# Kernel tuning notes

Hardware: AMD Instinct MI355X
Metric: run time of the kernel (lower is better)

Reference implementation:

```python
import jax, jax.numpy as jnp
import numpy as np

BATCH_SIZE = 8192   # args.batch_size
NUM_VIEWS = 2       # args.num_views
TEMPERATURE = 0.07  # args.loss_args['temperature']
FEAT_DIM = 256
N = (BATCH_SIZE // 2) * NUM_VIEWS  # rows of features


def _static_index_maps():
    # labels = sorted cat of num_views copies of arange(batch_size//2)
    labels = np.sort(np.tile(np.arange(BATCH_SIZE // 2), NUM_VIEWS))
    lab_mat = labels[None, :] == labels[:, None]          # (N, N) bool
    # off-diagonal column indices: for row i, columns [0..N-1] excluding i,
    # in ascending order (matches torch boolean-mask extraction order)
    j = np.arange(N - 1)
    cols = j[None, :] + (j[None, :] >= np.arange(N)[:, None])  # (N, N-1)
    lab_off = np.take_along_axis(lab_mat, cols, axis=1)        # (N, N-1) bool
    k = NUM_VIEWS - 1  # positives per row
    # stable sort puts positive positions first, preserving column order
    order = np.argsort(~lab_off, axis=1, kind='stable')
    pos_cols = order[:, :k]   # (N, k)
    neg_cols = order[:, k:]   # (N, N-1-k)
    return cols, pos_cols, neg_cols

_COLS, _POS_COLS, _NEG_COLS = _static_index_maps()


def setup_inputs() -> dict:
    key = jax.random.key(0)
    features = jax.random.normal(key, (N, FEAT_DIM), dtype=jnp.float32)
    return {"features": features}


def reference(features):
    # L2 normalize rows (F.normalize eps clamp)
    norm = jnp.maximum(jnp.linalg.norm(features, axis=1, keepdims=True), 1e-12)
    f = features / norm
    sim = f @ f.T                                            # (N, N)
    sim_off = jnp.take_along_axis(sim, jnp.asarray(_COLS), axis=1)       # (N, N-1)
    positives = jnp.take_along_axis(sim_off, jnp.asarray(_POS_COLS), axis=1)
    negatives = jnp.take_along_axis(sim_off, jnp.asarray(_NEG_COLS), axis=1)
    logits = jnp.concatenate([positives, negatives], axis=1) / TEMPERATURE
    # CrossEntropyLoss with target class 0 for every row
    loss = jnp.mean(-jax.nn.log_softmax(logits, axis=1)[:, 0])
    return loss
```

## Files before the change

### kernel.cpp

```cpp
#include <hip/hip_runtime.h>
#include <stdint.h>

#define N_ROWS 8192
#define FEAT   256
#define YSPLIT 32
#define CPB    (N_ROWS / YSPLIT)

typedef __bf16 bf16x8 __attribute__((ext_vector_type(8)));
typedef float  f32x4  __attribute__((ext_vector_type(4)));

__device__ __forceinline__ unsigned short f2bf(float x) {
    union { float f; uint32_t u; } v; v.f = x;
    uint32_t u = v.u;
    return (unsigned short)((u + 0x7FFFu + ((u >> 16) & 1u)) >> 16);
}

__global__ void knorm(const float* __restrict__ feat,
                      unsigned short* __restrict__ fb,
                      float* __restrict__ pos) {
    __shared__ float ex[4][FEAT];
    int wave = threadIdx.x >> 6;
    int lane = threadIdx.x & 63;
    int row  = blockIdx.x * 4 + wave;
    float4 v = ((const float4*)(feat + row * FEAT))[lane];
    float ss = v.x*v.x + v.y*v.y + v.z*v.z + v.w*v.w;
    #pragma unroll
    for (int off = 1; off < 64; off <<= 1) ss += __shfl_xor(ss, off);
    float inv = 1.0f / fmaxf(sqrtf(ss), 1e-12f);
    float4 o; o.x = v.x*inv; o.y = v.y*inv; o.z = v.z*inv; o.w = v.w*inv;
    ushort4 b;
    b.x = f2bf(o.x); b.y = f2bf(o.y); b.z = f2bf(o.z); b.w = f2bf(o.w);
    int sidx = (((lane >> 1) ^ (row & 7)) << 1) | (lane & 1);
    ((ushort4*)(fb + row * FEAT))[sidx] = b;
    ((float4*)ex[wave])[lane] = o;
    __syncthreads();
    float4 p = ((float4*)ex[wave ^ 1])[lane];
    float d = o.x*p.x + o.y*p.y + o.z*p.z + o.w*p.w;
    #pragma unroll
    for (int off = 1; off < 64; off <<= 1) d += __shfl_xor(d, off);
    if (lane == 0) pos[row] = d;
}

__global__ __launch_bounds__(256, 1)
void kmain(const unsigned short* __restrict__ fb, float* __restrict__ partial) {
    const int t    = threadIdx.x;
    const int lane = t & 63;
    const int wave = t >> 6;
    const int quad = lane >> 4;
    const int l15  = lane & 15;
    const int rw    = blockIdx.x * 256 + wave * 64;
    const int cbase = blockIdx.y * CPB;
    const float Kc = 20.60992915555662f;

    bf16x8 af[4][8];
    #pragma unroll
    for (int rf = 0; rf < 4; ++rf)
        #pragma unroll
        for (int ks = 0; ks < 8; ++ks) {
            int row = rw + rf * 16 + l15;
            int ch  = (ks * 4 + quad) ^ (row & 7);
            af[rf][ks] = *(const bf16x8*)(fb + row * FEAT + ch * 8);
        }

    float lsum[4][4] = {{0.f,0.f,0.f,0.f},{0.f,0.f,0.f,0.f},
                        {0.f,0.f,0.f,0.f},{0.f,0.f,0.f,0.f}};

    #pragma unroll 2
    for (int g = 0; g < CPB / 16; ++g) {
        const int cg = cbase + g * 16;
        const int C  = cg + l15;
        const unsigned short* bp = fb + (size_t)(cg + l15) * FEAT;
        f32x4 ac0 = {0.f,0.f,0.f,0.f};
        f32x4 ac1 = {0.f,0.f,0.f,0.f};
        f32x4 ac2 = {0.f,0.f,0.f,0.f};
        f32x4 ac3 = {0.f,0.f,0.f,0.f};
        #pragma unroll
        for (int ks = 0; ks < 8; ++ks) {
            bf16x8 bv = *(const bf16x8*)(bp + (((ks * 4 + quad) ^ (l15 & 7)) * 8));
            ac0 = __builtin_amdgcn_mfma_f32_16x16x32_bf16(af[0][ks], bv, ac0, 0, 0, 0);
            ac1 = __builtin_amdgcn_mfma_f32_16x16x32_bf16(af[1][ks], bv, ac1, 0, 0, 0);
            ac2 = __builtin_amdgcn_mfma_f32_16x16x32_bf16(af[2][ks], bv, ac2, 0, 0, 0);
            ac3 = __builtin_amdgcn_mfma_f32_16x16x32_bf16(af[3][ks], bv, ac3, 0, 0, 0);
        }
        #pragma unroll
        for (int rf = 0; rf < 4; ++rf) {
            const int rb = rw + rf * 16;
            const bool dg = (cg == rb);
            const f32x4 ac = (rf == 0) ? ac0 : (rf == 1) ? ac1
                           : (rf == 2) ? ac2 : ac3;
            #pragma unroll
            for (int r = 0; r < 4; ++r) {
                float e = __builtin_amdgcn_exp2f(fmaf(ac[r], Kc, -Kc));
                if (dg && (rb + quad * 4 + r == C)) e = 0.f;
                lsum[rf][r] += e;
            }
        }
    }

    #pragma unroll
    for (int rf = 0; rf < 4; ++rf)
        #pragma unroll
        for (int r = 0; r < 4; ++r) {
            float v = lsum[rf][r];
            v += __shfl_xor(v, 1);
            v += __shfl_xor(v, 2);
            v += __shfl_xor(v, 4);
            v += __shfl_xor(v, 8);
            lsum[rf][r] = v;
        }
    if (l15 == 0) {
        #pragma unroll
        for (int rf = 0; rf < 4; ++rf)
            #pragma unroll
            for (int r = 0; r < 4; ++r) {
                int row = rw + rf * 16 + quad * 4 + r;
                partial[blockIdx.y * N_ROWS + row] = lsum[rf][r];
            }
    }
}

__global__ void kreduce(const float* __restrict__ partial,
                        const float* __restrict__ pos,
                        float* __restrict__ bsum) {
    __shared__ float red[4];
    int row  = blockIdx.x * 256 + threadIdx.x;
    int wave = threadIdx.x >> 6;
    int lane = threadIdx.x & 63;
    float L = 0.f;
    #pragma unroll
    for (int p = 0; p < YSPLIT; ++p) L += partial[p * N_ROWS + row];
    const float invT = 14.285714285714286f;
    float loss = invT * (1.0f - pos[row])
               + 0.6931471805599453f * __builtin_amdgcn_logf(L);
    #pragma unroll
    for (int off = 1; off < 64; off <<= 1) loss += __shfl_xor(loss, off);
    if (lane == 0) red[wave] = loss;
    __syncthreads();
    if (threadIdx.x == 0)
        bsum[blockIdx.x] = red[0] + red[1] + red[2] + red[3];
}

__global__ void kfinal(const float* __restrict__ bsum, float* __restrict__ out) {
    int lane = threadIdx.x;
    float v = (lane < 32) ? bsum[lane] : 0.f;
    #pragma unroll
    for (int off = 1; off < 32; off <<= 1) v += __shfl_xor(v, off);
    if (lane == 0) out[0] = v * (1.0f / 8192.0f);
}

extern "C" void kernel_launch(void* const* d_in, const int* in_sizes, int n_in,
                              void* d_out, int out_size, void* d_ws, size_t ws_size,
                              hipStream_t stream) {
    const float* feat = (const float*)d_in[0];
    float* out = (float*)d_out;
    char* ws = (char*)d_ws;
    unsigned short* fb      = (unsigned short*)ws;
    float*          partial = (float*)(ws + (4u << 20));
    float*          pos     = (float*)(ws + (5u << 20));
    float*          bsum    = (float*)(ws + (5u << 20) + (1u << 15));

    knorm<<<N_ROWS / 4, 256, 0, stream>>>(feat, fb, pos);
    kmain<<<dim3(32, YSPLIT), 256, 0, stream>>>(fb, partial);
    kreduce<<<N_ROWS / 256, 256, 0, stream>>>(partial, pos, bsum);
    kfinal<<<1, 64, 0, stream>>>(bsum, out);
}
```

Baseline: 109.3 us.

## Exploit similarity matrix symmetry by computing only upper-triangular block pairs

The kernel now launches one pair of half-blocks per upper-triangular (row-block, column-block) pair instead of covering the full N×N grid. Each off-diagonal tile contributes its row-wise exp sums to the row block and its column-wise exp sums to the column block. This roughly halves the MFMA and exp work. In exchange it adds column reductions through shared memory, a triangular index decode loop, and zero-filling of unused slots. kreduce now sums twice as many partial slots.

Result: slower. 128.5 us (+17.6%).

```diff
diff --git a/kernel.cpp b/kernel.cpp
--- a/kernel.cpp
+++ b/kernel.cpp
@@ -3,8 +3,10 @@
 
 #define N_ROWS 8192
 #define FEAT   256
-#define YSPLIT 32
-#define CPB    (N_ROWS / YSPLIT)
+#define RB     256
+#define NB     (N_ROWS / RB)
+#define NPAIR  (NB * (NB + 1) / 2)
+#define NSLOT  (2 * NB)
 
 typedef __bf16 bf16x8 __attribute__((ext_vector_type(8)));
 typedef float  f32x4  __attribute__((ext_vector_type(4)));
@@ -43,13 +45,22 @@
 
 __global__ __launch_bounds__(256, 1)
 void kmain(const unsigned short* __restrict__ fb, float* __restrict__ partial) {
+    __shared__ float colred[4][128];
     const int t    = threadIdx.x;
     const int lane = t & 63;
     const int wave = t >> 6;
     const int quad = lane >> 4;
     const int l15  = lane & 15;
-    const int rw    = blockIdx.x * 256 + wave * 64;
-    const int cbase = blockIdx.y * CPB;
+
+    const int pair = blockIdx.x >> 1;
+    const int h    = blockIdx.x & 1;
+    int a = 0, rem = pair;
+    while (rem >= NB - a) { rem -= NB - a; ++a; }
+    const int b = a + rem;
+    const bool isdiag = (a == b);
+
+    const int rw    = a * RB + wave * 64;
+    const int cbase = b * RB + h * 128;
     const float Kc = 20.60992915555662f;
 
     bf16x8 af[4][8];
@@ -64,9 +75,10 @@
 
     float lsum[4][4] = {{0.f,0.f,0.f,0.f},{0.f,0.f,0.f,0.f},
                         {0.f,0.f,0.f,0.f},{0.f,0.f,0.f,0.f}};
+    float cs[8] = {0.f,0.f,0.f,0.f,0.f,0.f,0.f,0.f};
 
     #pragma unroll 2
-    for (int g = 0; g < CPB / 16; ++g) {
+    for (int g = 0; g < 8; ++g) {
         const int cg = cbase + g * 16;
         const int C  = cg + l15;
         const unsigned short* bp = fb + (size_t)(cg + l15) * FEAT;
@@ -93,10 +105,12 @@
                 float e = __builtin_amdgcn_exp2f(fmaf(ac[r], Kc, -Kc));
                 if (dg && (rb + quad * 4 + r == C)) e = 0.f;
                 lsum[rf][r] += e;
+                cs[g] += e;
             }
         }
     }
 
+    const int rslot = 2 * b + h;
     #pragma unroll
     for (int rf = 0; rf < 4; ++rf)
         #pragma unroll
@@ -114,8 +128,25 @@
             #pragma unroll
             for (int r = 0; r < 4; ++r) {
                 int row = rw + rf * 16 + quad * 4 + r;
-                partial[blockIdx.y * N_ROWS + row] = lsum[rf][r];
+                partial[rslot * N_ROWS + row] = lsum[rf][r];
             }
+    }
+
+    #pragma unroll
+    for (int g = 0; g < 8; ++g) {
+        float v = cs[g];
+        v += __shfl_xor(v, 16);
+        v += __shfl_xor(v, 32);
+        if (lane < 16) colred[wave][g * 16 + l15] = v;
+    }
+    __syncthreads();
+    if (!isdiag && t < 128) {
+        float s = colred[0][t] + colred[1][t] + colred[2][t] + colred[3][t];
+        partial[(2 * a) * N_ROWS + b * RB + h * 128 + t] = s;
+    }
+    if (isdiag && h == 0) {
+        for (int j = 0; j < a; ++j)
+            partial[(2 * j + 1) * N_ROWS + a * RB + t] = 0.f;
     }
 }
 
@@ -128,7 +159,7 @@
     int lane = threadIdx.x & 63;
     float L = 0.f;
     #pragma unroll
-    for (int p = 0; p < YSPLIT; ++p) L += partial[p * N_ROWS + row];
+    for (int p = 0; p < NSLOT; ++p) L += partial[p * N_ROWS + row];
     const float invT = 14.285714285714286f;
     float loss = invT * (1.0f - pos[row])
                + 0.6931471805599453f * __builtin_amdgcn_logf(L);
@@ -156,11 +187,11 @@
     char* ws = (char*)d_ws;
     unsigned short* fb      = (unsigned short*)ws;
     float*          partial = (float*)(ws + (4u << 20));
-    float*          pos     = (float*)(ws + (5u << 20));
-    float*          bsum    = (float*)(ws + (5u << 20) + (1u << 15));
+    float*          pos     = (float*)(ws + (6u << 20));
+    float*          bsum    = (float*)(ws + (6u << 20) + (1u << 15));
 
     knorm<<<N_ROWS / 4, 256, 0, stream>>>(feat, fb, pos);
-    kmain<<<dim3(32, YSPLIT), 256, 0, stream>>>(fb, partial);
+    kmain<<<NPAIR * 2, 256, 0, stream>>>(fb, partial);
     kreduce<<<N_ROWS / 256, 256, 0, stream>>>(partial, pos, bsum);
     kfinal<<<1, 64, 0, stream>>>(bsum, out);
 }
```
